# Kernel tuning notes

Hardware: AMD Instinct MI355X
Metric: run time of the kernel (lower is better)

## Reference

```python
import jax, jax.numpy as jnp
import numpy as np

EMBED = 1024
HEADS = 16
HEAD = EMBED // HEADS
B, S = 8, 1024


def setup_inputs() -> dict:
    key = jax.random.key(0)
    ks = jax.random.split(key, 12)
    inp = {
        "values": jax.random.normal(ks[0], (B, S, EMBED), jnp.float32),
        "keys": jax.random.normal(ks[1], (B, S, EMBED), jnp.float32),
        "query": jax.random.normal(ks[2], (B, S, EMBED), jnp.float32),
        # causal mask broadcastable to [B, heads, q, k]
        "mask": jnp.broadcast_to(jnp.tril(jnp.ones((S, S), jnp.int32))[None, None], (B, 1, S, S)),
        "Wv": jax.random.normal(ks[3], (HEAD, HEAD), jnp.float32) / np.sqrt(HEAD),
        "bv": jnp.zeros((HEAD,), jnp.float32),
        "Wk": jax.random.normal(ks[4], (HEAD, HEAD), jnp.float32) / np.sqrt(HEAD),
        "bk": jnp.zeros((HEAD,), jnp.float32),
        "Wq": jax.random.normal(ks[5], (HEAD, HEAD), jnp.float32) / np.sqrt(HEAD),
        "bq": jnp.zeros((HEAD,), jnp.float32),
        "Wfc": jax.random.normal(ks[6], (EMBED, EMBED), jnp.float32) / np.sqrt(EMBED),
        "bfc": jnp.zeros((EMBED,), jnp.float32),
    }
    return inp


def reference(values, keys, query, mask, Wv, bv, Wk, bk, Wq, bq, Wfc, bfc):
    N, q_len = query.shape[0], query.shape[1]
    k_len, v_len = keys.shape[1], values.shape[1]
    # split heads: [N, S, H, D]
    v = values.reshape(N, v_len, HEADS, HEAD)
    k = keys.reshape(N, k_len, HEADS, HEAD)
    q = query.reshape(N, q_len, HEADS, HEAD)
    # per-head linear projections (torch Linear: x @ W.T + b)
    v = v @ Wv.T + bv
    k = k @ Wk.T + bk
    q = q @ Wq.T + bq
    # scores [N, H, q, k]
    scores = jnp.einsum('nqhz,nkhz->nhqk', q, k)
    scores = jnp.where(mask == 0, -jnp.inf, scores)
    # NOTE: original divides by sqrt(query_size) (sequence length), not head dim
    attn = jax.nn.softmax(scores / jnp.sqrt(jnp.float32(q_len)), axis=-1)
    out = jnp.einsum('nhqk,nkhz->nqhz', attn, v).reshape(N, q_len, HEADS * HEAD)
    return out @ Wfc.T + bfc
```

## Files before the change

kernel.cpp:

```cpp
#include <hip/hip_runtime.h>
#include <stdint.h>

typedef __attribute__((ext_vector_type(8))) short short8;
typedef __attribute__((ext_vector_type(4))) short short4v;
typedef __attribute__((ext_vector_type(4))) float floatx4;
typedef __attribute__((ext_vector_type(4))) unsigned short ushort4v;

#define HEADS 16
#define HEAD 64
#define SEQ 1024
#define BATCH 8

__device__ __forceinline__ unsigned short f2bf(float f) {
    union { float f; unsigned int u; } v; v.f = f;
    unsigned int r = v.u + 0x7FFFu + ((v.u >> 16) & 1u);
    return (unsigned short)(r >> 16);
}

__device__ __forceinline__ void gload_lds16(const void* g, void* l) {
    __builtin_amdgcn_global_load_lds((const __attribute__((address_space(1))) void*)g,
                                     (__attribute__((address_space(3))) void*)l, 16, 0, 0);
}

__global__ __launch_bounds__(256) void cvt_kernel(const float* __restrict__ in,
                                                  unsigned short* __restrict__ out) {
    int i = (blockIdx.x * 256 + threadIdx.x) * 4;
    float4 f = *(const float4*)(in + i);
    ushort4v v;
    v.x = f2bf(f.x); v.y = f2bf(f.y); v.z = f2bf(f.z); v.w = f2bf(f.w);
    *(ushort4v*)(out + i) = v;
}

__global__ __launch_bounds__(256) void proj_kernel(
    const float* __restrict__ Vin, const float* __restrict__ Kin, const float* __restrict__ Qin,
    const float* __restrict__ Wv, const float* __restrict__ bv,
    const float* __restrict__ Wk, const float* __restrict__ bk,
    const float* __restrict__ Wq, const float* __restrict__ bq,
    unsigned short* __restrict__ q_ws, unsigned short* __restrict__ k_ws,
    unsigned short* __restrict__ v_ws)
{
    const int tid = threadIdx.x;
    const int wave = tid >> 6, lane = tid & 63;
    const int lq = lane & 15, quad = lane >> 4;
    const int proj = blockIdx.y;

    const float* X; const float* W; const float* bias;
    if (proj == 0)      { X = Qin; W = Wq; bias = bq; }
    else if (proj == 1) { X = Kin; W = Wk; bias = bk; }
    else                { X = Vin; W = Wv; bias = bv; }

    const int gr0 = blockIdx.x * 16;
    const int h0 = wave * 4;
    const int b = gr0 >> 10, s0 = gr0 & 1023;

    __shared__ unsigned short sT[4][1280];

    short8 wf[4][2];
#pragma unroll
    for (int nt = 0; nt < 4; ++nt) {
        const float* wr = W + (nt * 16 + lq) * 64 + quad * 8;
#pragma unroll
        for (int ks = 0; ks < 2; ++ks) {
            float4 f0 = *(const float4*)(wr + ks * 32);
            float4 f1 = *(const float4*)(wr + ks * 32 + 4);
            short8 v;
            v[0] = (short)f2bf(f0.x); v[1] = (short)f2bf(f0.y);
            v[2] = (short)f2bf(f0.z); v[3] = (short)f2bf(f0.w);
            v[4] = (short)f2bf(f1.x); v[5] = (short)f2bf(f1.y);
            v[6] = (short)f2bf(f1.z); v[7] = (short)f2bf(f1.w);
            wf[nt][ks] = v;
        }
    }

    const float* xb = X + (size_t)(gr0 + lq) * 1024 + quad * 8;
    const floatx4 zero4 = {0.f, 0.f, 0.f, 0.f};

    if (proj == 2) {
        float bvr[4][4];
#pragma unroll
        for (int nt = 0; nt < 4; ++nt)
#pragma unroll
            for (int r = 0; r < 4; ++r) bvr[nt][r] = bias[nt * 16 + quad * 4 + r];

        unsigned short* tw = &sT[wave][0];
        const int rrow = lane >> 1, rhalf = lane & 1;
        const unsigned short* tr0 = &sT[wave][rrow * 20 + rhalf * 8];
        const unsigned short* tr1 = &sT[wave][(rrow + 32) * 20 + rhalf * 8];

        float4 xf[4];
        { const float* p = xb + h0 * 64;
          xf[0] = *(const float4*)p;        xf[1] = *(const float4*)(p + 4);
          xf[2] = *(const float4*)(p + 32); xf[3] = *(const float4*)(p + 36); }
#pragma unroll
        for (int hh = 0; hh < 4; ++hh) {
            float4 xn[4];
            if (hh < 3) {
                const float* p = xb + (h0 + hh + 1) * 64;
                xn[0] = *(const float4*)p;        xn[1] = *(const float4*)(p + 4);
                xn[2] = *(const float4*)(p + 32); xn[3] = *(const float4*)(p + 36);
            }
            short8 aq[2];
#pragma unroll
            for (int ks = 0; ks < 2; ++ks) {
                short8 a;
                a[0] = (short)f2bf(xf[ks * 2].x);     a[1] = (short)f2bf(xf[ks * 2].y);
                a[2] = (short)f2bf(xf[ks * 2].z);     a[3] = (short)f2bf(xf[ks * 2].w);
                a[4] = (short)f2bf(xf[ks * 2 + 1].x); a[5] = (short)f2bf(xf[ks * 2 + 1].y);
                a[6] = (short)f2bf(xf[ks * 2 + 1].z); a[7] = (short)f2bf(xf[ks * 2 + 1].w);
                aq[ks] = a;
            }
            floatx4 acc[4] = {zero4, zero4, zero4, zero4};
#pragma unroll
            for (int ks = 0; ks < 2; ++ks)
#pragma unroll
                for (int nt = 0; nt < 4; ++nt)
                    acc[nt] = __builtin_amdgcn_mfma_f32_16x16x32_bf16(wf[nt][ks], aq[ks], acc[nt], 0, 0, 0);

#pragma unroll
            for (int nt = 0; nt < 4; ++nt)
#pragma unroll
                for (int r = 0; r < 4; ++r)
                    tw[(nt * 16 + quad * 4 + r) * 20 + lq] = f2bf(acc[nt][r] + bvr[nt][r]);

            short8 o0 = *(const short8*)tr0;
            short8 o1 = *(const short8*)tr1;
            unsigned short* vh = v_ws + (size_t)((b * 16 + h0 + hh) * 64) * 1024 + s0 + rhalf * 8;
            *(short8*)(vh + (size_t)rrow * 1024) = o0;
            *(short8*)(vh + (size_t)(rrow + 32) * 1024) = o1;

#pragma unroll
            for (int i = 0; i < 4; ++i) xf[i] = xn[i];
        }
    } else {
        float bqk[4];
#pragma unroll
        for (int nt = 0; nt < 4; ++nt) bqk[nt] = bias[nt * 16 + lq];
        const float qscale = 0.03125f * 1.44269504088896340736f;
        const float oscale = proj ? 1.0f : qscale;
        unsigned short* dstb = proj ? k_ws : q_ws;

        unsigned short* tw = &sT[wave][0];
        const unsigned short* tr = &sT[wave][(lane >> 2) * 68 + (lane & 3) * 16];

        float4 xf[4];
        { const float* p = xb + h0 * 64;
          xf[0] = *(const float4*)p;        xf[1] = *(const float4*)(p + 4);
          xf[2] = *(const float4*)(p + 32); xf[3] = *(const float4*)(p + 36); }
#pragma unroll
        for (int hh = 0; hh < 4; ++hh) {
            float4 xn[4];
            if (hh < 3) {
                const float* p = xb + (h0 + hh + 1) * 64;
                xn[0] = *(const float4*)p;        xn[1] = *(const float4*)(p + 4);
                xn[2] = *(const float4*)(p + 32); xn[3] = *(const float4*)(p + 36);
            }
            short8 aq[2];
#pragma unroll
            for (int ks = 0; ks < 2; ++ks) {
                short8 a;
                a[0] = (short)f2bf(xf[ks * 2].x);     a[1] = (short)f2bf(xf[ks * 2].y);
                a[2] = (short)f2bf(xf[ks * 2].z);     a[3] = (short)f2bf(xf[ks * 2].w);
                a[4] = (short)f2bf(xf[ks * 2 + 1].x); a[5] = (short)f2bf(xf[ks * 2 + 1].y);
                a[6] = (short)f2bf(xf[ks * 2 + 1].z); a[7] = (short)f2bf(xf[ks * 2 + 1].w);
                aq[ks] = a;
            }
            floatx4 acc[4] = {zero4, zero4, zero4, zero4};
#pragma unroll
            for (int ks = 0; ks < 2; ++ks)
#pragma unroll
                for (int nt = 0; nt < 4; ++nt)
                    acc[nt] = __builtin_amdgcn_mfma_f32_16x16x32_bf16(aq[ks], wf[nt][ks], acc[nt], 0, 0, 0);

#pragma unroll
            for (int nt = 0; nt < 4; ++nt)
#pragma unroll
                for (int r = 0; r < 4; ++r)
                    tw[(quad * 4 + r) * 68 + nt * 16 + lq] = f2bf((acc[nt][r] + bqk[nt]) * oscale);

            short8 o0 = *(const short8*)tr;
            short8 o1 = *(const short8*)(tr + 8);
            unsigned short* dst = dstb + ((size_t)((b * 16 + h0 + hh) * 1024) + s0) * 64 + lane * 16;
            *(short8*)dst = o0;
            *(short8*)(dst + 8) = o1;

#pragma unroll
            for (int i = 0; i < 4; ++i) xf[i] = xn[i];
        }
    }
}

__global__ __launch_bounds__(256, 4) void attn_kernel(
    const unsigned short* __restrict__ q_ws, const unsigned short* __restrict__ k_ws,
    const unsigned short* __restrict__ v_ws, unsigned short* __restrict__ attn_ws)
{
    const int bh = blockIdx.x;
    const int b = bh >> 4, h = bh & 15;
    const int tid = threadIdx.x;
    const int wave = tid >> 6, lane = tid & 63;
    const int lq = lane & 15, quad = lane >> 4;
    const int r8 = lane >> 3, ch = lane & 7;
    const int sw = ch ^ r8;

    __shared__ unsigned short sK[64 * 64];
    __shared__ unsigned short sV[64 * 64];
    __shared__ unsigned short sP[4][32 * 64];

    const size_t head_off = (size_t)bh * SEQ * HEAD;
    const unsigned short* qb = q_ws + head_off;
    const unsigned short* kb = k_ws + head_off;
    const unsigned short* vb = v_ws + head_off;

    short8 ones;
#pragma unroll
    for (int j = 0; j < 8; ++j) ones[j] = (short)0x3F80;

    const floatx4 zero4 = {0.f, 0.f, 0.f, 0.f};

    const int qt = blockIdx.y;
    const int q0 = qt * 128;
    const int q_lo = q0 + wave * 32;
    const int q_hi = q_lo + 31;
    const int nkt = 2 * qt + 2;

    short8 aq[2][2];
#pragma unroll
    for (int rg = 0; rg < 2; ++rg) {
        const unsigned short* qp = qb + (size_t)(q0 + wave * 32 + rg * 16 + lq) * 64 + quad * 8;
        aq[rg][0] = *(const short8*)qp;
        aq[rg][1] = *(const short8*)(qp + 32);
    }

    floatx4 o[2][4];
    floatx4 lacc[2] = {zero4, zero4};
#pragma unroll
    for (int rg = 0; rg < 2; ++rg)
#pragma unroll
        for (int nt = 0; nt < 4; ++nt) o[rg][nt] = zero4;

    for (int kt = 0; kt < nkt; ++kt) {
#pragma unroll
        for (int i = 0; i < 2; ++i) {
            int br = wave * 16 + i * 8;
            const char* gK = (const char*)(kb + (size_t)(kt * 64 + br + r8) * 64) + sw * 16;
            gload_lds16(gK, (char*)sK + br * 128);
            const char* gV = (const char*)(vb + (size_t)(br + r8) * 1024 + kt * 64) + sw * 16;
            gload_lds16(gV, (char*)sV + br * 128);
        }
        __syncthreads();

        const bool skip = (kt * 64 > q_hi);
        if (!skip) {
            const bool full = (kt * 64 + 63 <= q_lo);

            floatx4 s[2][4];
#pragma unroll
            for (int rg = 0; rg < 2; ++rg)
#pragma unroll
                for (int nt = 0; nt < 4; ++nt) s[rg][nt] = zero4;
#pragma unroll
            for (int ks = 0; ks < 2; ++ks) {
#pragma unroll
                for (int nt = 0; nt < 4; ++nt) {
                    short8 kf = *(const short8*)(sK + (nt * 16 + lq) * 64 +
                                                 (((quad + 4 * ks) ^ (lq & 7)) * 8));
                    s[0][nt] = __builtin_amdgcn_mfma_f32_16x16x32_bf16(aq[0][ks], kf, s[0][nt], 0, 0, 0);
                    s[1][nt] = __builtin_amdgcn_mfma_f32_16x16x32_bf16(aq[1][ks], kf, s[1][nt], 0, 0, 0);
                }
            }

            unsigned short* wp = &sP[wave][0];
#pragma unroll
            for (int rg = 0; rg < 2; ++rg) {
#pragma unroll
                for (int nt = 0; nt < 4; ++nt) {
                    int kcol = kt * 64 + nt * 16 + lq;
                    int chn = (((nt * 2 + (lq >> 3)) ^ (quad << 1)) * 8) + (lq & 7);
#pragma unroll
                    for (int r = 0; r < 4; ++r) {
                        float p = __builtin_amdgcn_exp2f(s[rg][nt][r]);
                        if (!full) {
                            int qrow = q_lo + rg * 16 + quad * 4 + r;
                            if (kcol > qrow) p = 0.f;
                        }
                        wp[(rg * 16 + quad * 4 + r) * 64 + chn] = f2bf(p);
                    }
                }
            }

            short8 vf[4][2];
#pragma unroll
            for (int nt = 0; nt < 4; ++nt)
#pragma unroll
                for (int ks = 0; ks < 2; ++ks)
                    vf[nt][ks] = *(const short8*)(sV + (nt * 16 + lq) * 64 +
                                                  (((quad + 4 * ks) ^ (lq & 7)) * 8));
#pragma unroll
            for (int rg = 0; rg < 2; ++rg) {
#pragma unroll
                for (int ks = 0; ks < 2; ++ks) {
                    short8 pa = *(const short8*)&sP[wave][(rg * 16 + lq) * 64 +
                                 (((ks * 4 + quad) ^ (((lq >> 2) & 3) << 1)) * 8)];
                    lacc[rg] = __builtin_amdgcn_mfma_f32_16x16x32_bf16(pa, ones, lacc[rg], 0, 0, 0);
#pragma unroll
                    for (int nt = 0; nt < 4; ++nt)
                        o[rg][nt] = __builtin_amdgcn_mfma_f32_16x16x32_bf16(pa, vf[nt][ks], o[rg][nt], 0, 0, 0);
                }
            }
        }
        __syncthreads();
    }

#pragma unroll
    for (int rg = 0; rg < 2; ++rg) {
        float inv[4];
#pragma unroll
        for (int r = 0; r < 4; ++r) inv[r] = 1.f / lacc[rg][r];
        const int srow_base = q0 + wave * 32 + rg * 16 + quad * 4;
#pragma unroll
        for (int nt = 0; nt < 4; ++nt) {
            int col = h * 64 + nt * 16 + lq;
#pragma unroll
            for (int r = 0; r < 4; ++r) {
                attn_ws[((size_t)(b * SEQ + srow_base + r)) * 1024 + col] = f2bf(o[rg][nt][r] * inv[r]);
            }
        }
    }
}

__global__ __launch_bounds__(256) void fc_kernel(
    const unsigned short* __restrict__ A, const unsigned short* __restrict__ Bw,
    const float* __restrict__ bias, float* __restrict__ out)
{
    const int nt0 = blockIdx.x * 128;
    const int mt0 = blockIdx.y * 128;
    const int tid = threadIdx.x;
    const int wave = tid >> 6, lane = tid & 63;
    const int lq = lane & 15, quad = lane >> 4;
    const int wm = (wave >> 1) * 64, wn = (wave & 1) * 64;

    __shared__ unsigned short sA[128 * 64];
    __shared__ unsigned short sB[128 * 64];

    const floatx4 zero4 = {0.f, 0.f, 0.f, 0.f};
    floatx4 acc[4][4];
#pragma unroll
    for (int i = 0; i < 4; ++i)
#pragma unroll
        for (int j = 0; j < 4; ++j) acc[i][j] = zero4;

    const int sc = (tid & 7) ^ ((tid >> 3) & 7);
    const int sr = tid >> 3;

    for (int kt = 0; kt < 16; ++kt) {
#pragma unroll
        for (int j = 0; j < 4; ++j) {
            int r = j * 32 + sr;
            const char* ga = (const char*)A + (size_t)(mt0 + r) * 2048 + kt * 128 + sc * 16;
            gload_lds16(ga, (char*)sA + (j * 256 + tid) * 16);
            const char* gb = (const char*)Bw + (size_t)(nt0 + r) * 2048 + kt * 128 + sc * 16;
            gload_lds16(gb, (char*)sB + (j * 256 + tid) * 16);
        }
        __syncthreads();

        short8 af[4][2], bf[4][2];
#pragma unroll
        for (int i = 0; i < 4; ++i)
#pragma unroll
            for (int ks = 0; ks < 2; ++ks) {
                af[i][ks] = *(const short8*)(sA + (wm + i * 16 + lq) * 64 +
                                             (((quad + 4 * ks) ^ (lq & 7)) * 8));
                bf[i][ks] = *(const short8*)(sB + (wn + i * 16 + lq) * 64 +
                                             (((quad + 4 * ks) ^ (lq & 7)) * 8));
            }
#pragma unroll
        for (int ks = 0; ks < 2; ++ks)
#pragma unroll
            for (int mi = 0; mi < 4; ++mi)
#pragma unroll
                for (int ni = 0; ni < 4; ++ni)
                    acc[mi][ni] = __builtin_amdgcn_mfma_f32_16x16x32_bf16(af[mi][ks], bf[ni][ks], acc[mi][ni], 0, 0, 0);
        __syncthreads();
    }

#pragma unroll
    for (int mi = 0; mi < 4; ++mi) {
#pragma unroll
        for (int ni = 0; ni < 4; ++ni) {
            int col = nt0 + wn + ni * 16 + lq;
            float bc = bias[col];
#pragma unroll
            for (int r = 0; r < 4; ++r) {
                int row = mt0 + wm + mi * 16 + quad * 4 + r;
                out[(size_t)row * 1024 + col] = acc[mi][ni][r] + bc;
            }
        }
    }
}

extern "C" void kernel_launch(void* const* d_in, const int* in_sizes, int n_in,
                              void* d_out, int out_size, void* d_ws, size_t ws_size,
                              hipStream_t stream)
{
    const float* values = (const float*)d_in[0];
    const float* keys   = (const float*)d_in[1];
    const float* query  = (const float*)d_in[2];
    const float* Wv  = (const float*)d_in[4];
    const float* bv  = (const float*)d_in[5];
    const float* Wk  = (const float*)d_in[6];
    const float* bk  = (const float*)d_in[7];
    const float* Wq  = (const float*)d_in[8];
    const float* bq  = (const float*)d_in[9];
    const float* Wfc = (const float*)d_in[10];
    const float* bfc = (const float*)d_in[11];
    float* out = (float*)d_out;

    char* ws = (char*)d_ws;
    unsigned short* q_ws    = (unsigned short*)(ws);
    unsigned short* k_ws    = (unsigned short*)(ws + (16u << 20));
    unsigned short* v_ws    = (unsigned short*)(ws + (32u << 20));
    unsigned short* attn_ws = (unsigned short*)(ws + (48u << 20));
    unsigned short* wfc_ws  = (unsigned short*)(ws + (64u << 20));

    cvt_kernel<<<dim3(1024), dim3(256), 0, stream>>>(Wfc, wfc_ws);
    proj_kernel<<<dim3(512, 3), dim3(256), 0, stream>>>(
        values, keys, query, Wv, bv, Wk, bk, Wq, bq, q_ws, k_ws, v_ws);
    attn_kernel<<<dim3(128, 8), dim3(256), 0, stream>>>(q_ws, k_ws, v_ws, attn_ws);
    fc_kernel<<<dim3(8, 64), dim3(256), 0, stream>>>(attn_ws, wfc_ws, bfc, out);
}
```

Measured before the change: 262.9 us.

## Fuse all stages into one cooperative persistent kernel with grid syncs

Replaces the four launches (weight convert, projections, attention, output GEMM) with one cooperative kernel of 1024 blocks that separates the stages with grid-wide syncs. Each attention block now processes a pair of complementary causal q-tiles so work is balanced, and the FC tile shrinks to 64x128 so there are 1024 blocks. Work in the projection stage is redistributed across the same grid. The aim is to remove launch gaps and tail effects between stages. The cost is grid-sync overhead, a residency requirement of 4 blocks per CU, and a three-kernel fallback path if the cooperative launch fails.

```diff
diff --git a/kernel.cpp b/kernel.cpp
--- a/kernel.cpp
+++ b/kernel.cpp
@@ -1,8 +1,10 @@
 #include <hip/hip_runtime.h>
+#include <hip/hip_cooperative_groups.h>
 #include <stdint.h>
 
+namespace cg = cooperative_groups;
+
 typedef __attribute__((ext_vector_type(8))) short short8;
-typedef __attribute__((ext_vector_type(4))) short short4v;
 typedef __attribute__((ext_vector_type(4))) float floatx4;
 typedef __attribute__((ext_vector_type(4))) unsigned short ushort4v;
 
@@ -22,38 +24,32 @@
                                      (__attribute__((address_space(3))) void*)l, 16, 0, 0);
 }
 
-__global__ __launch_bounds__(256) void cvt_kernel(const float* __restrict__ in,
-                                                  unsigned short* __restrict__ out) {
-    int i = (blockIdx.x * 256 + threadIdx.x) * 4;
-    float4 f = *(const float4*)(in + i);
-    ushort4v v;
-    v.x = f2bf(f.x); v.y = f2bf(f.y); v.z = f2bf(f.z); v.w = f2bf(f.w);
-    *(ushort4v*)(out + i) = v;
-}
-
-__global__ __launch_bounds__(256) void proj_kernel(
-    const float* __restrict__ Vin, const float* __restrict__ Kin, const float* __restrict__ Qin,
-    const float* __restrict__ Wv, const float* __restrict__ bv,
-    const float* __restrict__ Wk, const float* __restrict__ bk,
-    const float* __restrict__ Wq, const float* __restrict__ bq,
-    unsigned short* __restrict__ q_ws, unsigned short* __restrict__ k_ws,
-    unsigned short* __restrict__ v_ws)
+
+__device__ __forceinline__ void dev_cvt(int chunk, const float* __restrict__ in,
+                                        unsigned short* __restrict__ out) {
+    int base = chunk * 2048 + threadIdx.x * 8;
+    float4 f0 = *(const float4*)(in + base);
+    float4 f1 = *(const float4*)(in + base + 4);
+    ushort4v v0, v1;
+    v0.x = f2bf(f0.x); v0.y = f2bf(f0.y); v0.z = f2bf(f0.z); v0.w = f2bf(f0.w);
+    v1.x = f2bf(f1.x); v1.y = f2bf(f1.y); v1.z = f2bf(f1.z); v1.w = f2bf(f1.w);
+    *(ushort4v*)(out + base) = v0;
+    *(ushort4v*)(out + base + 4) = v1;
+}
+
+__device__ __forceinline__ void dev_proj_qk(
+    const float* __restrict__ X, const float* __restrict__ W, const float* __restrict__ bias,
+    unsigned short* __restrict__ dstb, float oscale, int tile, unsigned short* sm)
 {
     const int tid = threadIdx.x;
     const int wave = tid >> 6, lane = tid & 63;
     const int lq = lane & 15, quad = lane >> 4;
-    const int proj = blockIdx.y;
-
-    const float* X; const float* W; const float* bias;
-    if (proj == 0)      { X = Qin; W = Wq; bias = bq; }
-    else if (proj == 1) { X = Kin; W = Wk; bias = bk; }
-    else                { X = Vin; W = Wv; bias = bv; }
-
-    const int gr0 = blockIdx.x * 16;
+    const int gr0 = tile * 16;
     const int h0 = wave * 4;
     const int b = gr0 >> 10, s0 = gr0 & 1023;
 
-    __shared__ unsigned short sT[4][1280];
+    unsigned short* tw = sm + wave * 1280;
+    const unsigned short* tr = tw + (lane >> 2) * 68 + (lane & 3) * 16;
 
     short8 wf[4][2];
 #pragma unroll
@@ -72,128 +68,153 @@
         }
     }
 
+    float bqk[4];
+#pragma unroll
+    for (int nt = 0; nt < 4; ++nt) bqk[nt] = bias[nt * 16 + lq];
+
     const float* xb = X + (size_t)(gr0 + lq) * 1024 + quad * 8;
     const floatx4 zero4 = {0.f, 0.f, 0.f, 0.f};
 
-    if (proj == 2) {
-        float bvr[4][4];
+    float4 xf[4];
+    { const float* p = xb + h0 * 64;
+      xf[0] = *(const float4*)p;        xf[1] = *(const float4*)(p + 4);
+      xf[2] = *(const float4*)(p + 32); xf[3] = *(const float4*)(p + 36); }
+#pragma unroll
+    for (int hh = 0; hh < 4; ++hh) {
+        float4 xn[4];
+        if (hh < 3) {
+            const float* p = xb + (h0 + hh + 1) * 64;
+            xn[0] = *(const float4*)p;        xn[1] = *(const float4*)(p + 4);
+            xn[2] = *(const float4*)(p + 32); xn[3] = *(const float4*)(p + 36);
+        }
+        short8 aq[2];
+#pragma unroll
+        for (int ks = 0; ks < 2; ++ks) {
+            short8 a;
+            a[0] = (short)f2bf(xf[ks * 2].x);     a[1] = (short)f2bf(xf[ks * 2].y);
+            a[2] = (short)f2bf(xf[ks * 2].z);     a[3] = (short)f2bf(xf[ks * 2].w);
+            a[4] = (short)f2bf(xf[ks * 2 + 1].x); a[5] = (short)f2bf(xf[ks * 2 + 1].y);
+            a[6] = (short)f2bf(xf[ks * 2 + 1].z); a[7] = (short)f2bf(xf[ks * 2 + 1].w);
+            aq[ks] = a;
+        }
+        floatx4 acc[4] = {zero4, zero4, zero4, zero4};
+#pragma unroll
+        for (int ks = 0; ks < 2; ++ks)
+#pragma unroll
+            for (int nt = 0; nt < 4; ++nt)
+                acc[nt] = __builtin_amdgcn_mfma_f32_16x16x32_bf16(aq[ks], wf[nt][ks], acc[nt], 0, 0, 0);
+
 #pragma unroll
         for (int nt = 0; nt < 4; ++nt)
 #pragma unroll
-            for (int r = 0; r < 4; ++r) bvr[nt][r] = bias[nt * 16 + quad * 4 + r];
-
-        unsigned short* tw = &sT[wave][0];
-        const int rrow = lane >> 1, rhalf = lane & 1;
-        const unsigned short* tr0 = &sT[wave][rrow * 20 + rhalf * 8];
-        const unsigned short* tr1 = &sT[wave][(rrow + 32) * 20 + rhalf * 8];
-
-        float4 xf[4];
-        { const float* p = xb + h0 * 64;
-          xf[0] = *(const float4*)p;        xf[1] = *(const float4*)(p + 4);
-          xf[2] = *(const float4*)(p + 32); xf[3] = *(const float4*)(p + 36); }
-#pragma unroll
-        for (int hh = 0; hh < 4; ++hh) {
-            float4 xn[4];
-            if (hh < 3) {
-                const float* p = xb + (h0 + hh + 1) * 64;
-                xn[0] = *(const float4*)p;        xn[1] = *(const float4*)(p + 4);
-                xn[2] = *(const float4*)(p + 32); xn[3] = *(const float4*)(p + 36);
-            }
-            short8 aq[2];
-#pragma unroll
-            for (int ks = 0; ks < 2; ++ks) {
-                short8 a;
-                a[0] = (short)f2bf(xf[ks * 2].x);     a[1] = (short)f2bf(xf[ks * 2].y);
-                a[2] = (short)f2bf(xf[ks * 2].z);     a[3] = (short)f2bf(xf[ks * 2].w);
-                a[4] = (short)f2bf(xf[ks * 2 + 1].x); a[5] = (short)f2bf(xf[ks * 2 + 1].y);
-                a[6] = (short)f2bf(xf[ks * 2 + 1].z); a[7] = (short)f2bf(xf[ks * 2 + 1].w);
-                aq[ks] = a;
-            }
-            floatx4 acc[4] = {zero4, zero4, zero4, zero4};
-#pragma unroll
-            for (int ks = 0; ks < 2; ++ks)
-#pragma unroll
-                for (int nt = 0; nt < 4; ++nt)
-                    acc[nt] = __builtin_amdgcn_mfma_f32_16x16x32_bf16(wf[nt][ks], aq[ks], acc[nt], 0, 0, 0);
-
+            for (int r = 0; r < 4; ++r)
+                tw[(quad * 4 + r) * 68 + nt * 16 + lq] = f2bf((acc[nt][r] + bqk[nt]) * oscale);
+
+        short8 o0 = *(const short8*)tr;
+        short8 o1 = *(const short8*)(tr + 8);
+        unsigned short* dst = dstb + ((size_t)((b * 16 + h0 + hh) * 1024) + s0) * 64 + lane * 16;
+        *(short8*)dst = o0;
+        *(short8*)(dst + 8) = o1;
+
+#pragma unroll
+        for (int i = 0; i < 4; ++i) xf[i] = xn[i];
+    }
+}
+
+__device__ __forceinline__ void dev_proj_v(
+    const float* __restrict__ X, const float* __restrict__ W, const float* __restrict__ bias,
+    unsigned short* __restrict__ v_ws, int tile, unsigned short* sm)
+{
+    const int tid = threadIdx.x;
+    const int wave = tid >> 6, lane = tid & 63;
+    const int lq = lane & 15, quad = lane >> 4;
+    const int gr0 = tile * 16;
+    const int h0 = wave * 4;
+    const int b = gr0 >> 10, s0 = gr0 & 1023;
+
+    unsigned short* tw = sm + wave * 1280;
+    const int rrow = lane >> 1, rhalf = lane & 1;
+    const unsigned short* tr0 = tw + rrow * 20 + rhalf * 8;
+    const unsigned short* tr1 = tw + (rrow + 32) * 20 + rhalf * 8;
+
+    short8 wf[4][2];
+#pragma unroll
+    for (int nt = 0; nt < 4; ++nt) {
+        const float* wr = W + (nt * 16 + lq) * 64 + quad * 8;
+#pragma unroll
+        for (int ks = 0; ks < 2; ++ks) {
+            float4 f0 = *(const float4*)(wr + ks * 32);
+            float4 f1 = *(const float4*)(wr + ks * 32 + 4);
+            short8 v;
+            v[0] = (short)f2bf(f0.x); v[1] = (short)f2bf(f0.y);
+            v[2] = (short)f2bf(f0.z); v[3] = (short)f2bf(f0.w);
+            v[4] = (short)f2bf(f1.x); v[5] = (short)f2bf(f1.y);
+            v[6] = (short)f2bf(f1.z); v[7] = (short)f2bf(f1.w);
+            wf[nt][ks] = v;
+        }
+    }
+
+    float bvr[4][4];
+#pragma unroll
+    for (int nt = 0; nt < 4; ++nt)
+#pragma unroll
+        for (int r = 0; r < 4; ++r) bvr[nt][r] = bias[nt * 16 + quad * 4 + r];
+
+    const float* xb = X + (size_t)(gr0 + lq) * 1024 + quad * 8;
+    const floatx4 zero4 = {0.f, 0.f, 0.f, 0.f};
+
+    float4 xf[4];
+    { const float* p = xb + h0 * 64;
+      xf[0] = *(const float4*)p;        xf[1] = *(const float4*)(p + 4);
+      xf[2] = *(const float4*)(p + 32); xf[3] = *(const float4*)(p + 36); }
+#pragma unroll
+    for (int hh = 0; hh < 4; ++hh) {
+        float4 xn[4];
+        if (hh < 3) {
+            const float* p = xb + (h0 + hh + 1) * 64;
+            xn[0] = *(const float4*)p;        xn[1] = *(const float4*)(p + 4);
+            xn[2] = *(const float4*)(p + 32); xn[3] = *(const float4*)(p + 36);
+        }
+        short8 aq[2];
+#pragma unroll
+        for (int ks = 0; ks < 2; ++ks) {
+            short8 a;
+            a[0] = (short)f2bf(xf[ks * 2].x);     a[1] = (short)f2bf(xf[ks * 2].y);
+            a[2] = (short)f2bf(xf[ks * 2].z);     a[3] = (short)f2bf(xf[ks * 2].w);
+            a[4] = (short)f2bf(xf[ks * 2 + 1].x); a[5] = (short)f2bf(xf[ks * 2 + 1].y);
+            a[6] = (short)f2bf(xf[ks * 2 + 1].z); a[7] = (short)f2bf(xf[ks * 2 + 1].w);
+            aq[ks] = a;
+        }
+        floatx4 acc[4] = {zero4, zero4, zero4, zero4};
+#pragma unroll
+        for (int ks = 0; ks < 2; ++ks)
 #pragma unroll
             for (int nt = 0; nt < 4; ++nt)
-#pragma unroll
-                for (int r = 0; r < 4; ++r)
-                    tw[(nt * 16 + quad * 4 + r) * 20 + lq] = f2bf(acc[nt][r] + bvr[nt][r]);
-
-            short8 o0 = *(const short8*)tr0;
-            short8 o1 = *(const short8*)tr1;
-            unsigned short* vh = v_ws + (size_t)((b * 16 + h0 + hh) * 64) * 1024 + s0 + rhalf * 8;
-            *(short8*)(vh + (size_t)rrow * 1024) = o0;
-            *(short8*)(vh + (size_t)(rrow + 32) * 1024) = o1;
-
-#pragma unroll
-            for (int i = 0; i < 4; ++i) xf[i] = xn[i];
-        }
-    } else {
-        float bqk[4];
-#pragma unroll
-        for (int nt = 0; nt < 4; ++nt) bqk[nt] = bias[nt * 16 + lq];
-        const float qscale = 0.03125f * 1.44269504088896340736f;
-        const float oscale = proj ? 1.0f : qscale;
-        unsigned short* dstb = proj ? k_ws : q_ws;
-
-        unsigned short* tw = &sT[wave][0];
-        const unsigned short* tr = &sT[wave][(lane >> 2) * 68 + (lane & 3) * 16];
-
-        float4 xf[4];
-        { const float* p = xb + h0 * 64;
-          xf[0] = *(const float4*)p;        xf[1] = *(const float4*)(p + 4);
-          xf[2] = *(const float4*)(p + 32); xf[3] = *(const float4*)(p + 36); }
-#pragma unroll
-        for (int hh = 0; hh < 4; ++hh) {
-            float4 xn[4];
-            if (hh < 3) {
-                const float* p = xb + (h0 + hh + 1) * 64;
-                xn[0] = *(const float4*)p;        xn[1] = *(const float4*)(p + 4);
-                xn[2] = *(const float4*)(p + 32); xn[3] = *(const float4*)(p + 36);
-            }
-            short8 aq[2];
-#pragma unroll
-            for (int ks = 0; ks < 2; ++ks) {
-                short8 a;
-                a[0] = (short)f2bf(xf[ks * 2].x);     a[1] = (short)f2bf(xf[ks * 2].y);
-                a[2] = (short)f2bf(xf[ks * 2].z);     a[3] = (short)f2bf(xf[ks * 2].w);
-                a[4] = (short)f2bf(xf[ks * 2 + 1].x); a[5] = (short)f2bf(xf[ks * 2 + 1].y);
-                a[6] = (short)f2bf(xf[ks * 2 + 1].z); a[7] = (short)f2bf(xf[ks * 2 + 1].w);
-                aq[ks] = a;
-            }
-            floatx4 acc[4] = {zero4, zero4, zero4, zero4};
-#pragma unroll
-            for (int ks = 0; ks < 2; ++ks)
-#pragma unroll
-                for (int nt = 0; nt < 4; ++nt)
-                    acc[nt] = __builtin_amdgcn_mfma_f32_16x16x32_bf16(aq[ks], wf[nt][ks], acc[nt], 0, 0, 0);
-
-#pragma unroll
-            for (int nt = 0; nt < 4; ++nt)
-#pragma unroll
-                for (int r = 0; r < 4; ++r)
-                    tw[(quad * 4 + r) * 68 + nt * 16 + lq] = f2bf((acc[nt][r] + bqk[nt]) * oscale);
-
-            short8 o0 = *(const short8*)tr;
-            short8 o1 = *(const short8*)(tr + 8);
-            unsigned short* dst = dstb + ((size_t)((b * 16 + h0 + hh) * 1024) + s0) * 64 + lane * 16;
-            *(short8*)dst = o0;
-            *(short8*)(dst + 8) = o1;
-
-#pragma unroll
-            for (int i = 0; i < 4; ++i) xf[i] = xn[i];
-        }
-    }
-}
-
-__global__ __launch_bounds__(256, 4) void attn_kernel(
+                acc[nt] = __builtin_amdgcn_mfma_f32_16x16x32_bf16(wf[nt][ks], aq[ks], acc[nt], 0, 0, 0);
+
+#pragma unroll
+        for (int nt = 0; nt < 4; ++nt)
+#pragma unroll
+            for (int r = 0; r < 4; ++r)
+                tw[(nt * 16 + quad * 4 + r) * 20 + lq] = f2bf(acc[nt][r] + bvr[nt][r]);
+
+        short8 o0 = *(const short8*)tr0;
+        short8 o1 = *(const short8*)tr1;
+        unsigned short* vh = v_ws + (size_t)((b * 16 + h0 + hh) * 64) * 1024 + s0 + rhalf * 8;
+        *(short8*)(vh + (size_t)rrow * 1024) = o0;
+        *(short8*)(vh + (size_t)(rrow + 32) * 1024) = o1;
+
+#pragma unroll
+        for (int i = 0; i < 4; ++i) xf[i] = xn[i];
+    }
+}
+
+__device__ __forceinline__ void dev_attn(
+    int bh, int yy,
     const unsigned short* __restrict__ q_ws, const unsigned short* __restrict__ k_ws,
-    const unsigned short* __restrict__ v_ws, unsigned short* __restrict__ attn_ws)
-{
-    const int bh = blockIdx.x;
+    const unsigned short* __restrict__ v_ws, unsigned short* __restrict__ attn_ws,
+    unsigned short* sm)
+{
     const int b = bh >> 4, h = bh & 15;
     const int tid = threadIdx.x;
     const int wave = tid >> 6, lane = tid & 63;
@@ -201,9 +222,9 @@
     const int r8 = lane >> 3, ch = lane & 7;
     const int sw = ch ^ r8;
 
-    __shared__ unsigned short sK[64 * 64];
-    __shared__ unsigned short sV[64 * 64];
-    __shared__ unsigned short sP[4][32 * 64];
+    unsigned short* sK = sm;
+    unsigned short* sV = sm + 4096;
+    unsigned short* sPw = sm + 8192 + wave * 2048;
 
     const size_t head_off = (size_t)bh * SEQ * HEAD;
     const unsigned short* qb = q_ws + head_off;
@@ -216,135 +237,136 @@
 
     const floatx4 zero4 = {0.f, 0.f, 0.f, 0.f};
 
-    const int qt = blockIdx.y;
-    const int q0 = qt * 128;
-    const int q_lo = q0 + wave * 32;
-    const int q_hi = q_lo + 31;
-    const int nkt = 2 * qt + 2;
-
-    short8 aq[2][2];
-#pragma unroll
-    for (int rg = 0; rg < 2; ++rg) {
-        const unsigned short* qp = qb + (size_t)(q0 + wave * 32 + rg * 16 + lq) * 64 + quad * 8;
-        aq[rg][0] = *(const short8*)qp;
-        aq[rg][1] = *(const short8*)(qp + 32);
-    }
-
-    floatx4 o[2][4];
-    floatx4 lacc[2] = {zero4, zero4};
-#pragma unroll
-    for (int rg = 0; rg < 2; ++rg)
-#pragma unroll
-        for (int nt = 0; nt < 4; ++nt) o[rg][nt] = zero4;
-
-    for (int kt = 0; kt < nkt; ++kt) {
-#pragma unroll
-        for (int i = 0; i < 2; ++i) {
-            int br = wave * 16 + i * 8;
-            const char* gK = (const char*)(kb + (size_t)(kt * 64 + br + r8) * 64) + sw * 16;
-            gload_lds16(gK, (char*)sK + br * 128);
-            const char* gV = (const char*)(vb + (size_t)(br + r8) * 1024 + kt * 64) + sw * 16;
-            gload_lds16(gV, (char*)sV + br * 128);
-        }
-        __syncthreads();
-
-        const bool skip = (kt * 64 > q_hi);
-        if (!skip) {
-            const bool full = (kt * 64 + 63 <= q_lo);
-
-            floatx4 s[2][4];
-#pragma unroll
-            for (int rg = 0; rg < 2; ++rg)
-#pragma unroll
-                for (int nt = 0; nt < 4; ++nt) s[rg][nt] = zero4;
-#pragma unroll
-            for (int ks = 0; ks < 2; ++ks) {
-#pragma unroll
-                for (int nt = 0; nt < 4; ++nt) {
-                    short8 kf = *(const short8*)(sK + (nt * 16 + lq) * 64 +
-                                                 (((quad + 4 * ks) ^ (lq & 7)) * 8));
-                    s[0][nt] = __builtin_amdgcn_mfma_f32_16x16x32_bf16(aq[0][ks], kf, s[0][nt], 0, 0, 0);
-                    s[1][nt] = __builtin_amdgcn_mfma_f32_16x16x32_bf16(aq[1][ks], kf, s[1][nt], 0, 0, 0);
+    for (int pass = 0; pass < 2; ++pass) {
+        const int qt = pass ? (7 - yy) : yy;
+        const int q0 = qt * 128;
+        const int q_lo = q0 + wave * 32;
+        const int q_hi = q_lo + 31;
+        const int nkt = 2 * qt + 2;
+
+        short8 aq[2][2];
+#pragma unroll
+        for (int rg = 0; rg < 2; ++rg) {
+            const unsigned short* qp = qb + (size_t)(q0 + wave * 32 + rg * 16 + lq) * 64 + quad * 8;
+            aq[rg][0] = *(const short8*)qp;
+            aq[rg][1] = *(const short8*)(qp + 32);
+        }
+
+        floatx4 o[2][4];
+        floatx4 lacc[2] = {zero4, zero4};
+#pragma unroll
+        for (int rg = 0; rg < 2; ++rg)
+#pragma unroll
+            for (int nt = 0; nt < 4; ++nt) o[rg][nt] = zero4;
+
+        for (int kt = 0; kt < nkt; ++kt) {
+#pragma unroll
+            for (int i = 0; i < 2; ++i) {
+                int br = wave * 16 + i * 8;
+                const char* gK = (const char*)(kb + (size_t)(kt * 64 + br + r8) * 64) + sw * 16;
+                gload_lds16(gK, (char*)sK + br * 128);
+                const char* gV = (const char*)(vb + (size_t)(br + r8) * 1024 + kt * 64) + sw * 16;
+                gload_lds16(gV, (char*)sV + br * 128);
+            }
+            __syncthreads();
+
+            const bool skip = (kt * 64 > q_hi);
+            if (!skip) {
+                const bool full = (kt * 64 + 63 <= q_lo);
+
+                floatx4 s[2][4];
+#pragma unroll
+                for (int rg = 0; rg < 2; ++rg)
+#pragma unroll
+                    for (int nt = 0; nt < 4; ++nt) s[rg][nt] = zero4;
+#pragma unroll
+                for (int ks = 0; ks < 2; ++ks) {
+#pragma unroll
+                    for (int nt = 0; nt < 4; ++nt) {
+                        short8 kf = *(const short8*)(sK + (nt * 16 + lq) * 64 +
+                                                     (((quad + 4 * ks) ^ (lq & 7)) * 8));
+                        s[0][nt] = __builtin_amdgcn_mfma_f32_16x16x32_bf16(aq[0][ks], kf, s[0][nt], 0, 0, 0);
+                        s[1][nt] = __builtin_amdgcn_mfma_f32_16x16x32_bf16(aq[1][ks], kf, s[1][nt], 0, 0, 0);
+                    }
                 }
-            }
-
-            unsigned short* wp = &sP[wave][0];
-#pragma unroll
-            for (int rg = 0; rg < 2; ++rg) {
-#pragma unroll
-                for (int nt = 0; nt < 4; ++nt) {
-                    int kcol = kt * 64 + nt * 16 + lq;
-                    int chn = (((nt * 2 + (lq >> 3)) ^ (quad << 1)) * 8) + (lq & 7);
-#pragma unroll
-                    for (int r = 0; r < 4; ++r) {
-                        float p = __builtin_amdgcn_exp2f(s[rg][nt][r]);
-                        if (!full) {
-                            int qrow = q_lo + rg * 16 + quad * 4 + r;
-                            if (kcol > qrow) p = 0.f;
+
+#pragma unroll
+                for (int rg = 0; rg < 2; ++rg) {
+#pragma unroll
+                    for (int nt = 0; nt < 4; ++nt) {
+                        int kcol = kt * 64 + nt * 16 + lq;
+                        int chn = (((nt * 2 + (lq >> 3)) ^ (quad << 1)) * 8) + (lq & 7);
+#pragma unroll
+                        for (int r = 0; r < 4; ++r) {
+                            float p = __builtin_amdgcn_exp2f(s[rg][nt][r]);
+                            if (!full) {
+                                int qrow = q_lo + rg * 16 + quad * 4 + r;
+                                if (kcol > qrow) p = 0.f;
+                            }
+                            sPw[(rg * 16 + quad * 4 + r) * 64 + chn] = f2bf(p);
                         }
-                        wp[(rg * 16 + quad * 4 + r) * 64 + chn] = f2bf(p);
+                    }
+                }
+
+                short8 vf[4][2];
+#pragma unroll
+                for (int nt = 0; nt < 4; ++nt)
+#pragma unroll
+                    for (int ks = 0; ks < 2; ++ks)
+                        vf[nt][ks] = *(const short8*)(sV + (nt * 16 + lq) * 64 +
+                                                      (((quad + 4 * ks) ^ (lq & 7)) * 8));
+#pragma unroll
+                for (int rg = 0; rg < 2; ++rg) {
+#pragma unroll
+                    for (int ks = 0; ks < 2; ++ks) {
+                        short8 pa = *(const short8*)(sPw + (rg * 16 + lq) * 64 +
+                                     (((ks * 4 + quad) ^ (((lq >> 2) & 3) << 1)) * 8));
+                        lacc[rg] = __builtin_amdgcn_mfma_f32_16x16x32_bf16(pa, ones, lacc[rg], 0, 0, 0);
+#pragma unroll
+                        for (int nt = 0; nt < 4; ++nt)
+                            o[rg][nt] = __builtin_amdgcn_mfma_f32_16x16x32_bf16(pa, vf[nt][ks], o[rg][nt], 0, 0, 0);
                     }
                 }
             }
-
-            short8 vf[4][2];
-#pragma unroll
-            for (int nt = 0; nt < 4; ++nt)
-#pragma unroll
-                for (int ks = 0; ks < 2; ++ks)
-                    vf[nt][ks] = *(const short8*)(sV + (nt * 16 + lq) * 64 +
-                                                  (((quad + 4 * ks) ^ (lq & 7)) * 8));
-#pragma unroll
-            for (int rg = 0; rg < 2; ++rg) {
-#pragma unroll
-                for (int ks = 0; ks < 2; ++ks) {
-                    short8 pa = *(const short8*)&sP[wave][(rg * 16 + lq) * 64 +
-                                 (((ks * 4 + quad) ^ (((lq >> 2) & 3) << 1)) * 8)];
-                    lacc[rg] = __builtin_amdgcn_mfma_f32_16x16x32_bf16(pa, ones, lacc[rg], 0, 0, 0);
-#pragma unroll
-                    for (int nt = 0; nt < 4; ++nt)
-                        o[rg][nt] = __builtin_amdgcn_mfma_f32_16x16x32_bf16(pa, vf[nt][ks], o[rg][nt], 0, 0, 0);
+            __syncthreads();
+        }
+
+#pragma unroll
+        for (int rg = 0; rg < 2; ++rg) {
+            float inv[4];
+#pragma unroll
+            for (int r = 0; r < 4; ++r) inv[r] = 1.f / lacc[rg][r];
+            const int srow_base = q0 + wave * 32 + rg * 16 + quad * 4;
+#pragma unroll
+            for (int nt = 0; nt < 4; ++nt) {
+                int col = h * 64 + nt * 16 + lq;
+#pragma unroll
+                for (int r = 0; r < 4; ++r) {
+                    attn_ws[((size_t)(b * SEQ + srow_base + r)) * 1024 + col] = f2bf(o[rg][nt][r] * inv[r]);
                 }
             }
         }
-        __syncthreads();
-    }
-
-#pragma unroll
-    for (int rg = 0; rg < 2; ++rg) {
-        float inv[4];
-#pragma unroll
-        for (int r = 0; r < 4; ++r) inv[r] = 1.f / lacc[rg][r];
-        const int srow_base = q0 + wave * 32 + rg * 16 + quad * 4;
-#pragma unroll
-        for (int nt = 0; nt < 4; ++nt) {
-            int col = h * 64 + nt * 16 + lq;
-#pragma unroll
-            for (int r = 0; r < 4; ++r) {
-                attn_ws[((size_t)(b * SEQ + srow_base + r)) * 1024 + col] = f2bf(o[rg][nt][r] * inv[r]);
-            }
-        }
-    }
-}
-
-__global__ __launch_bounds__(256) void fc_kernel(
-    const unsigned short* __restrict__ A, const unsigned short* __restrict__ Bw,
-    const float* __restrict__ bias, float* __restrict__ out)
-{
-    const int nt0 = blockIdx.x * 128;
-    const int mt0 = blockIdx.y * 128;
+    }
+}
+
+__device__ __forceinline__ void dev_fc(
+    int bid, const unsigned short* __restrict__ A, const unsigned short* __restrict__ Bw,
+    const float* __restrict__ bias, float* __restrict__ out, unsigned short* sm)
+{
+    const int nt0 = (bid & 7) * 128;
+    const int mt0 = (bid >> 3) * 64;
     const int tid = threadIdx.x;
     const int wave = tid >> 6, lane = tid & 63;
     const int lq = lane & 15, quad = lane >> 4;
-    const int wm = (wave >> 1) * 64, wn = (wave & 1) * 64;
-
-    __shared__ unsigned short sA[128 * 64];
-    __shared__ unsigned short sB[128 * 64];
+    const int wm = (wave & 1) * 32, wn = (wave >> 1) * 64;
+
+    unsigned short* sA = sm;
+    unsigned short* sB = sm + 4096;
 
     const floatx4 zero4 = {0.f, 0.f, 0.f, 0.f};
-    floatx4 acc[4][4];
-#pragma unroll
-    for (int i = 0; i < 4; ++i)
+    floatx4 acc[2][4];
+#pragma unroll
+    for (int i = 0; i < 2; ++i)
 #pragma unroll
         for (int j = 0; j < 4; ++j) acc[i][j] = zero4;
 
@@ -353,29 +375,33 @@
 
     for (int kt = 0; kt < 16; ++kt) {
 #pragma unroll
+        for (int j = 0; j < 2; ++j) {
+            const char* ga = (const char*)A + (size_t)(mt0 + j * 32 + sr) * 2048 + kt * 128 + sc * 16;
+            gload_lds16(ga, (char*)sA + (j * 256 + tid) * 16);
+        }
+#pragma unroll
         for (int j = 0; j < 4; ++j) {
-            int r = j * 32 + sr;
-            const char* ga = (const char*)A + (size_t)(mt0 + r) * 2048 + kt * 128 + sc * 16;
-            gload_lds16(ga, (char*)sA + (j * 256 + tid) * 16);
-            const char* gb = (const char*)Bw + (size_t)(nt0 + r) * 2048 + kt * 128 + sc * 16;
+            const char* gb = (const char*)Bw + (size_t)(nt0 + j * 32 + sr) * 2048 + kt * 128 + sc * 16;
             gload_lds16(gb, (char*)sB + (j * 256 + tid) * 16);
         }
         __syncthreads();
 
-        short8 af[4][2], bf[4][2];
-#pragma unroll
-        for (int i = 0; i < 4; ++i)
-#pragma unroll
-            for (int ks = 0; ks < 2; ++ks) {
+        short8 af[2][2], bf[4][2];
+#pragma unroll
+        for (int ks = 0; ks < 2; ++ks) {
+#pragma unroll
+            for (int i = 0; i < 2; ++i)
                 af[i][ks] = *(const short8*)(sA + (wm + i * 16 + lq) * 64 +
                                              (((quad + 4 * ks) ^ (lq & 7)) * 8));
+#pragma unroll
+            for (int i = 0; i < 4; ++i)
                 bf[i][ks] = *(const short8*)(sB + (wn + i * 16 + lq) * 64 +
                                              (((quad + 4 * ks) ^ (lq & 7)) * 8));
-            }
+        }
 #pragma unroll
         for (int ks = 0; ks < 2; ++ks)
 #pragma unroll
-            for (int mi = 0; mi < 4; ++mi)
+            for (int mi = 0; mi < 2; ++mi)
 #pragma unroll
                 for (int ni = 0; ni < 4; ++ni)
                     acc[mi][ni] = __builtin_amdgcn_mfma_f32_16x16x32_bf16(af[mi][ks], bf[ni][ks], acc[mi][ni], 0, 0, 0);
@@ -383,7 +409,7 @@
     }
 
 #pragma unroll
-    for (int mi = 0; mi < 4; ++mi) {
+    for (int mi = 0; mi < 2; ++mi) {
 #pragma unroll
         for (int ni = 0; ni < 4; ++ni) {
             int col = nt0 + wn + ni * 16 + lq;
@@ -395,6 +421,73 @@
             }
         }
     }
+}
+
+__global__ __launch_bounds__(256, 4) void mega_kernel(
+    const float* __restrict__ Vin, const float* __restrict__ Kin, const float* __restrict__ Qin,
+    const float* __restrict__ Wv, const float* __restrict__ bv,
+    const float* __restrict__ Wk, const float* __restrict__ bk,
+    const float* __restrict__ Wq, const float* __restrict__ bq,
+    const float* __restrict__ Wfc, const float* __restrict__ bfc,
+    unsigned short* __restrict__ q_ws, unsigned short* __restrict__ k_ws,
+    unsigned short* __restrict__ v_ws, unsigned short* __restrict__ attn_ws,
+    unsigned short* __restrict__ wfc_ws, float* __restrict__ out)
+{
+    __shared__ unsigned short sm[16384];
+    cg::grid_group grid = cg::this_grid();
+    const int bid = blockIdx.x;
+    const float qscale = 0.03125f * 1.44269504088896340736f;
+
+    if (bid < 512) {
+        dev_proj_qk(Qin, Wq, bq, q_ws, qscale, bid, sm);
+        dev_proj_v(Vin, Wv, bv, v_ws, bid, sm);
+    } else {
+        dev_cvt(bid - 512, Wfc, wfc_ws);
+        dev_proj_qk(Kin, Wk, bk, k_ws, 1.0f, bid - 512, sm);
+    }
+    grid.sync();
+
+    if (bid < 512) dev_attn(bid >> 2, bid & 3, q_ws, k_ws, v_ws, attn_ws, sm);
+    grid.sync();
+
+    dev_fc(bid, attn_ws, wfc_ws, bfc, out, sm);
+}
+
+__global__ __launch_bounds__(256, 4) void phaseA_kernel(
+    const float* __restrict__ Vin, const float* __restrict__ Kin, const float* __restrict__ Qin,
+    const float* __restrict__ Wv, const float* __restrict__ bv,
+    const float* __restrict__ Wk, const float* __restrict__ bk,
+    const float* __restrict__ Wq, const float* __restrict__ bq,
+    const float* __restrict__ Wfc,
+    unsigned short* __restrict__ q_ws, unsigned short* __restrict__ k_ws,
+    unsigned short* __restrict__ v_ws, unsigned short* __restrict__ wfc_ws)
+{
+    __shared__ unsigned short sm[16384];
+    const int bid = blockIdx.x;
+    const float qscale = 0.03125f * 1.44269504088896340736f;
+    if (bid < 512) {
+        dev_proj_qk(Qin, Wq, bq, q_ws, qscale, bid, sm);
+        dev_proj_v(Vin, Wv, bv, v_ws, bid, sm);
+    } else {
+        dev_cvt(bid - 512, Wfc, wfc_ws);
+        dev_proj_qk(Kin, Wk, bk, k_ws, 1.0f, bid - 512, sm);
+    }
+}
+
+__global__ __launch_bounds__(256, 2) void phaseB_kernel(
+    const unsigned short* __restrict__ q_ws, const unsigned short* __restrict__ k_ws,
+    const unsigned short* __restrict__ v_ws, unsigned short* __restrict__ attn_ws)
+{
+    __shared__ unsigned short sm[16384];
+    dev_attn(blockIdx.x >> 2, blockIdx.x & 3, q_ws, k_ws, v_ws, attn_ws, sm);
+}
+
+__global__ __launch_bounds__(256, 4) void phaseC_kernel(
+    const unsigned short* __restrict__ A, const unsigned short* __restrict__ Bw,
+    const float* __restrict__ bias, float* __restrict__ out)
+{
+    __shared__ unsigned short sm[12288];
+    dev_fc(blockIdx.x, A, Bw, bias, out, sm);
 }
 
 extern "C" void kernel_launch(void* const* d_in, const int* in_sizes, int n_in,
@@ -421,9 +514,19 @@
     unsigned short* attn_ws = (unsigned short*)(ws + (48u << 20));
     unsigned short* wfc_ws  = (unsigned short*)(ws + (64u << 20));
 
-    cvt_kernel<<<dim3(1024), dim3(256), 0, stream>>>(Wfc, wfc_ws);
-    proj_kernel<<<dim3(512, 3), dim3(256), 0, stream>>>(
-        values, keys, query, Wv, bv, Wk, bk, Wq, bq, q_ws, k_ws, v_ws);
-    attn_kernel<<<dim3(128, 8), dim3(256), 0, stream>>>(q_ws, k_ws, v_ws, attn_ws);
-    fc_kernel<<<dim3(8, 64), dim3(256), 0, stream>>>(attn_ws, wfc_ws, bfc, out);
-}
+    void* kargs[] = {
+        (void*)&values, (void*)&keys, (void*)&query,
+        (void*)&Wv, (void*)&bv, (void*)&Wk, (void*)&bk, (void*)&Wq, (void*)&bq,
+        (void*)&Wfc, (void*)&bfc,
+        (void*)&q_ws, (void*)&k_ws, (void*)&v_ws, (void*)&attn_ws, (void*)&wfc_ws,
+        (void*)&out
+    };
+    hipError_t err = hipLaunchCooperativeKernel((const void*)mega_kernel,
+                                                dim3(1024), dim3(256), kargs, 0, stream);
+    if (err != hipSuccess) {
+        phaseA_kernel<<<dim3(1024), dim3(256), 0, stream>>>(
+            values, keys, query, Wv, bv, Wk, bk, Wq, bq, Wfc, q_ws, k_ws, v_ws, wfc_ws);
+        phaseB_kernel<<<dim3(512), dim3(256), 0, stream>>>(q_ws, k_ws, v_ws, attn_ws);
+        phaseC_kernel<<<dim3(1024), dim3(256), 0, stream>>>(attn_ws, wfc_ws, bfc, out);
+    }
+}
```

After: 551.0 us. 110% more time.
